# Kernel tuning notes

Measured on AMD Instinct MI355X. Metric: run time of the kernel, lower is better.

## Reference

```python
import jax, jax.numpy as jnp
import numpy as np

B, T, D = 4, 2048, 1024
H = int(D * 8.0)          # SwiGLU hidden (ffn_ratio=8)
SPARSITY = 0.95
THRESHOLD = 0.05          # PLIF firing threshold
PLIF_TAU = 2.5            # PLIF tau init
ALPHA = 2.0               # atan surrogate sharpness
EPS = 1e-6


@jax.custom_vjp
def spike(x):
    # Heaviside in fwd; atan surrogate gradient in bwd.
    return (x > 0).astype(x.dtype)

def _spike_fwd(x):
    return spike(x), x

def _spike_bwd(x, g):
    return (g * (ALPHA / 2.0) / (1.0 + (jnp.pi / 2.0 * ALPHA * x) ** 2),)

spike.defvjp(_spike_fwd, _spike_bwd)


def rmsnorm(x, w):
    return x * jax.lax.rsqrt(jnp.mean(x * x, axis=-1, keepdims=True) + EPS) * w


def setup_inputs() -> dict:
    key = jax.random.key(0)
    ks = jax.random.split(key, 12)
    f32 = jnp.float32
    return {
        "x": jax.random.normal(ks[0], (B, T, D), f32),
        "ln1_w": jnp.ones((D,), f32),
        "liq_win": (jax.random.normal(ks[1], (D, D), f32) / np.float32(np.sqrt(D))),
        "liq_wrec": (jax.random.normal(ks[2], (D, D), f32) / np.float32(np.sqrt(D))),
        "liq_b": jnp.zeros((D,), f32),
        "liq_tau": jnp.ones((D,), f32),  # softplus -> per-unit time constant
        "plif_w": jnp.asarray(-np.log(PLIF_TAU - 1.0), f32),  # sigmoid(w)=1/tau
        "syn_w": jax.random.normal(ks[3], (D, D), f32) * 0.02,
        "gate_w": jax.random.normal(ks[4], (D, D), f32) * 0.01,
        "gate_b": jnp.zeros((D,), f32),
        "ln2_w": jnp.ones((D,), f32),
        "ffn_wg": jax.random.normal(ks[5], (H, D), f32) * 0.02,
        "ffn_wu": jax.random.normal(ks[6], (H, D), f32) * 0.02,
        "ffn_wd": jax.random.normal(ks[7], (D, H), f32) * (0.02 / np.float32(np.sqrt(2.0))),
        "syn_mask": (jax.random.uniform(ks[8], (D, D)) > SPARSITY),  # bool, fixed
    }


def reference(x, ln1_w, liq_win, liq_wrec, liq_b, liq_tau, plif_w, syn_w,
              gate_w, gate_b, ln2_w, ffn_wg, ffn_wu, ffn_wd, syn_mask):
    # --- pre-norm ---
    a = rmsnorm(x, ln1_w)                       # (B,T,D)
    a_t = jnp.swapaxes(a, 0, 1)                 # (T,B,D)

    # --- LiquidCell: liquid time-constant recurrence over T ---
    tau = jax.nn.softplus(liq_tau)              # (D,) per-unit time constant

    def liq_step(h, xt):
        pre = xt @ liq_win.T + h @ liq_wrec.T + liq_b
        h = h + (jnp.tanh(pre) - h) / tau
        return h, h

    h0 = jnp.zeros((x.shape[0], D), x.dtype)
    _, h_seq = jax.lax.scan(liq_step, h0, a_t)  # (T,B,D)

    # --- PLIFCell.forward_seq: parametric LIF, subtract reset ---
    decay = jax.nn.sigmoid(plif_w)              # scalar = 1/tau_plif

    def plif_step(v, ht):
        v = v + decay * (ht - v)
        s = spike(v - THRESHOLD)
        v = v - s * THRESHOLD                   # reset='subtract'
        return v, s

    _, s_seq = jax.lax.scan(plif_step, jnp.zeros_like(h0), h_seq)
    s = jnp.swapaxes(s_seq, 0, 1)               # (B,T,D) spikes

    # --- SparseSynapse * sigmoid gate ---
    w_eff = syn_w * syn_mask.astype(syn_w.dtype)
    gated = (s @ w_eff.T) * jax.nn.sigmoid(s @ gate_w.T + gate_b)
    x = x + gated                               # dropout=0 -> identity

    # --- SwiGLU FFN residual ---
    y = rmsnorm(x, ln2_w)
    ff = (jax.nn.silu(y @ ffn_wg.T) * (y @ ffn_wu.T)) @ ffn_wd.T
    return x + ff
```

## Files before the change

kernel.cpp:

```cpp
#include <hip/hip_runtime.h>
#include <hip/hip_bf16.h>

#define TT 2048
#define DIM 1024
#define HFF 8192
#define NBATCH 4
#define PWG 32
#define THRESH 0.05f

typedef __bf16 bf16x8 __attribute__((ext_vector_type(8)));
typedef float f32x4 __attribute__((ext_vector_type(4)));

__device__ __forceinline__ unsigned short f2bf(float f) {
    __hip_bfloat16 h = __float2bfloat16(f);
    return __builtin_bit_cast(unsigned short, h);
}
__device__ __forceinline__ float bf2f(unsigned short u) {
    return __bfloat162float(__builtin_bit_cast(__hip_bfloat16, u));
}
__device__ __forceinline__ bf16x8 ldf(const unsigned short* p) {
    return *reinterpret_cast<const bf16x8*>(p);
}

__device__ __forceinline__ void ld2x4_mall(const float* p0, const float* p1,
                                           f32x4* a, f32x4* b) {
    asm volatile("global_load_dwordx4 %0, %2, off sc0 sc1\n\t"
                 "global_load_dwordx4 %1, %3, off sc0 sc1\n\t"
                 "s_waitcnt vmcnt(0)"
                 : "=&v"(*a), "=&v"(*b) : "v"(p0), "v"(p1) : "memory");
}

__device__ __forceinline__ void gload_lds16(const void* g, void* l) {
    __builtin_amdgcn_global_load_lds(
        (const __attribute__((address_space(1))) unsigned int*)g,
        (__attribute__((address_space(3))) unsigned int*)l, 16, 0, 0);
}

__global__ void maskprobe_k(const unsigned int* mask_words, int* flag) {
    __shared__ int allok;
    if (threadIdx.x == 0) allok = 1;
    __syncthreads();
    int ok = 1;
    for (int i = 0; i < 16; ++i) {
        unsigned int w = mask_words[threadIdx.x * 16 + i];
        if (w > 1u) ok = 0;
    }
    if (!ok) atomicAnd(&allok, 0);
    __syncthreads();
    if (threadIdx.x == 0) flag[0] = allok;
}

__global__ void weff_k(const float* __restrict__ synw, const void* __restrict__ mask,
                       const int* __restrict__ flag, unsigned short* __restrict__ dst) {
    const int isInt = flag[0];
    const int n = DIM * DIM;
    for (int i = blockIdx.x * 256 + threadIdx.x; i < n; i += gridDim.x * 256) {
        bool m;
        if (isInt) m = ((const int*)mask)[i] != 0;
        else       m = ((const unsigned char*)mask)[i] != 0;
        dst[i] = f2bf(m ? synw[i] : 0.f);
    }
}

__global__ void conv_k(const float* __restrict__ src, unsigned short* __restrict__ dst, int n) {
    for (int i = blockIdx.x * 256 + threadIdx.x; i < n; i += gridDim.x * 256)
        dst[i] = f2bf(src[i]);
}

__global__ void split_k(const float* __restrict__ src, unsigned short* __restrict__ hi,
                        unsigned short* __restrict__ lo, int n) {
    for (int i = blockIdx.x * 256 + threadIdx.x; i < n; i += gridDim.x * 256) {
        float v = src[i];
        unsigned short h = f2bf(v);
        hi[i] = h;
        lo[i] = f2bf(v - bf2f(h));
    }
}

__global__ void spkexp_k(const unsigned int* __restrict__ spk, unsigned short* __restrict__ sbf) {
    const int i = blockIdx.x * 256 + threadIdx.x;
    const unsigned int w = spk[i];
    const int d = i & 1023, t32 = (i >> 10) & 63, b = i >> 16;
    const size_t base = ((size_t)b * TT + (size_t)t32 * 32) * DIM + d;
    #pragma unroll
    for (int j = 0; j < 32; ++j)
        sbf[base + (size_t)j * DIM] = ((w >> j) & 1u) ? (unsigned short)0x3F80 : (unsigned short)0;
}

template <bool SPLIT>
__global__ void rms_k(const float* __restrict__ xin, const float* __restrict__ w,
                      unsigned short* __restrict__ hi, unsigned short* __restrict__ lo) {
    const int row = blockIdx.x;
    const int tid = threadIdx.x;
    const float4 xv = *reinterpret_cast<const float4*>(xin + (size_t)row * DIM + tid * 4);
    float ss = xv.x * xv.x + xv.y * xv.y + xv.z * xv.z + xv.w * xv.w;
    #pragma unroll
    for (int m = 1; m <= 32; m <<= 1) ss += __shfl_xor(ss, m);
    __shared__ float red[5];
    if ((tid & 63) == 0) red[tid >> 6] = ss;
    __syncthreads();
    if (tid == 0) {
        float s = red[0] + red[1] + red[2] + red[3];
        red[4] = 1.f / sqrtf(s * (1.f / DIM) + 1e-6f);
    }
    __syncthreads();
    const float scale = red[4];
    const float wv[4] = {w[tid*4], w[tid*4+1], w[tid*4+2], w[tid*4+3]};
    const float xa[4] = {xv.x, xv.y, xv.z, xv.w};
    #pragma unroll
    for (int i = 0; i < 4; ++i) {
        float v = xa[i] * scale * wv[i];
        unsigned short h = f2bf(v);
        hi[(size_t)row * DIM + tid * 4 + i] = h;
        if constexpr (SPLIT) lo[(size_t)row * DIM + tid * 4 + i] = f2bf(v - bf2f(h));
    }
}

template <int EPI>
__global__ __launch_bounds__(256, 1) void gemm2_k(
    const unsigned short* __restrict__ A,  const unsigned short* __restrict__ Alo,
    const unsigned short* __restrict__ B1, const unsigned short* __restrict__ B1lo,
    const unsigned short* __restrict__ B2,
    const float* __restrict__ aux1, const float* __restrict__ aux2,
    float* __restrict__ outf, unsigned short* __restrict__ outbf,
    int N, int K) {
    constexpr bool HILO = (EPI == 0);
    constexpr bool DUAL = (EPI == 1 || EPI == 2);
    __shared__ unsigned short sA[128 * 64];
    __shared__ unsigned short sB1[128 * 64];
    __shared__ unsigned short sAlo[HILO ? 128 * 64 : 8];
    __shared__ unsigned short sBlo[HILO ? 128 * 64 : 8];
    __shared__ unsigned short sB2[DUAL ? 128 * 64 : 8];
    const int lane = threadIdx.x & 63;
    const int wv = threadIdx.x >> 6;
    const int l15 = lane & 15, l4 = lane >> 4;
    const long row0 = (long)blockIdx.y * 128;
    const long col0 = (long)blockIdx.x * 128;
    const int wr = wv >> 1, wc = wv & 1;
    const int crow = lane >> 3;
    const int cbyte = (lane & 7) * 16;
    f32x4 acc[4][4];
    f32x4 acc2[DUAL ? 4 : 1][DUAL ? 4 : 1];
    #pragma unroll
    for (int i = 0; i < 4; ++i)
        #pragma unroll
        for (int j = 0; j < 4; ++j) {
            acc[i][j] = (f32x4){0.f, 0.f, 0.f, 0.f};
            if constexpr (DUAL) acc2[i][j] = (f32x4){0.f, 0.f, 0.f, 0.f};
        }
    for (int kt = 0; kt < K; kt += 64) {
        #pragma unroll
        for (int i = 0; i < 4; ++i) {
            const int chunk = wv * 4 + i;
            const int trow = chunk * 8 + crow;
            const size_t goffA = ((row0 + trow) * (size_t)K + kt) * 2 + cbyte;
            const size_t goffB = ((col0 + trow) * (size_t)K + kt) * 2 + cbyte;
            gload_lds16((const char*)A + goffA, (char*)sA + chunk * 1024);
            gload_lds16((const char*)B1 + goffB, (char*)sB1 + chunk * 1024);
            if constexpr (HILO) {
                gload_lds16((const char*)Alo + goffA, (char*)sAlo + chunk * 1024);
                gload_lds16((const char*)B1lo + goffB, (char*)sBlo + chunk * 1024);
            }
            if constexpr (DUAL)
                gload_lds16((const char*)B2 + goffB, (char*)sB2 + chunk * 1024);
        }
        __syncthreads();
        #pragma unroll
        for (int kk2 = 0; kk2 < 64; kk2 += 32) {
            bf16x8 af[4], bf_[4], al[4], bl[4], b2f[4];
            #pragma unroll
            for (int i = 0; i < 4; ++i) {
                const int ao = (wr * 64 + i * 16 + l15) * 64 + kk2 + l4 * 8;
                const int bo = (wc * 64 + i * 16 + l15) * 64 + kk2 + l4 * 8;
                af[i]  = ldf(sA + ao);
                bf_[i] = ldf(sB1 + bo);
                if constexpr (HILO) { al[i] = ldf(sAlo + ao); bl[i] = ldf(sBlo + bo); }
                if constexpr (DUAL) b2f[i] = ldf(sB2 + bo);
            }
            #pragma unroll
            for (int i = 0; i < 4; ++i)
                #pragma unroll
                for (int j = 0; j < 4; ++j) {
                    acc[i][j] = __builtin_amdgcn_mfma_f32_16x16x32_bf16(af[i], bf_[j], acc[i][j], 0, 0, 0);
                    if constexpr (HILO) {
                        acc[i][j] = __builtin_amdgcn_mfma_f32_16x16x32_bf16(af[i], bl[j], acc[i][j], 0, 0, 0);
                        acc[i][j] = __builtin_amdgcn_mfma_f32_16x16x32_bf16(al[i], bf_[j], acc[i][j], 0, 0, 0);
                    }
                    if constexpr (DUAL)
                        acc2[i][j] = __builtin_amdgcn_mfma_f32_16x16x32_bf16(af[i], b2f[j], acc2[i][j], 0, 0, 0);
                }
        }
        __syncthreads();
    }
    #pragma unroll
    for (int i = 0; i < 4; ++i) {
        #pragma unroll
        for (int r = 0; r < 4; ++r) {
            const long row = row0 + wr * 64 + i * 16 + l4 * 4 + r;
            #pragma unroll
            for (int j = 0; j < 4; ++j) {
                const long col = col0 + wc * 64 + j * 16 + l15;
                float v = acc[i][j][r];
                if constexpr (EPI == 0) {
                    int m = (int)row;
                    int bb = m >> 11, tt = m & 2047;
                    outf[((size_t)(tt * NBATCH + bb)) * DIM + col] = v + aux1[col];
                } else if constexpr (EPI == 1) {
                    size_t idx = (size_t)row * N + col;
                    float gg = acc2[i][j][r] + aux2[col];
                    outf[idx] = aux1[idx] + v * (1.f / (1.f + expf(-gg)));
                } else if constexpr (EPI == 2) {
                    size_t idx = (size_t)row * N + col;
                    float u = acc2[i][j][r];
                    outbf[idx] = f2bf((v / (1.f + expf(-v))) * u);
                } else {
                    size_t idx = (size_t)row * N + col;
                    outf[idx] = aux1[idx] + v;
                }
            }
        }
    }
}

__global__ __launch_bounds__(512, 1) void recur_k(
    const float* __restrict__ wrec, const float* __restrict__ U,
    const float* __restrict__ liqtau, const float* __restrict__ plifw,
    float* __restrict__ hg, int* __restrict__ flags, unsigned int* __restrict__ spk) {
    const int tid = threadIdx.x;
    const int wg = blockIdx.x;
    const int g = tid >> 6;
    const int L = tid & 63;
    const int kp = L;
    const int d0 = wg * 32 + g * 4;

    float wreg[4][16];
    #pragma unroll
    for (int d = 0; d < 4; ++d) {
        const float* wr = wrec + (size_t)(d0 + d) * DIM + kp * 16;
        #pragma unroll
        for (int q = 0; q < 4; ++q) {
            f32x4 w4 = *reinterpret_cast<const f32x4*>(wr + q * 4);
            wreg[d][q*4+0] = w4[0]; wreg[d][q*4+1] = w4[1];
            wreg[d][q*4+2] = w4[2]; wreg[d][q*4+3] = w4[3];
        }
    }

    __shared__ float hl[4 * 1088];
    for (int i = tid; i < 4 * 1088; i += 512) hl[i] = 0.f;

    const int od = L >> 2, ob = L & 3;
    const int odim = d0 + od;
    const bool own = (L < 16);
    float hq = 0.f, vq = 0.f, tauv = 1.f;
    unsigned smask = 0u;
    const float decay = 1.f / (1.f + expf(-plifw[0]));
    if (own) {
        float lt = liqtau[odim];
        tauv = (lt > 20.f) ? lt : log1pf(expf(lt));
    }
    const int sel1 = L & 1, sel2 = (L >> 1) & 1, sel4 = (L >> 2) & 1, sel8 = (L >> 3) & 1;

    int cb[4];
    #pragma unroll
    for (int b = 0; b < 4; ++b)
        cb[b] = b * 1088 + (kp >> 2) * 68 + (kp & 3) * 16;
    __syncthreads();

    for (int t = 0; t < TT; ++t) {
        float uvp = 0.f;
        if (own) uvp = U[((size_t)t * NBATCH + ob) * DIM + odim];

        float a[16];
        #pragma unroll
        for (int v = 0; v < 16; ++v) a[v] = 0.f;
        #pragma unroll
        for (int q = 0; q < 4; ++q) {
            const f32x4 h0 = *reinterpret_cast<const f32x4*>(hl + cb[0] + q * 4);
            const f32x4 h1 = *reinterpret_cast<const f32x4*>(hl + cb[1] + q * 4);
            const f32x4 h2 = *reinterpret_cast<const f32x4*>(hl + cb[2] + q * 4);
            const f32x4 h3 = *reinterpret_cast<const f32x4*>(hl + cb[3] + q * 4);
            #pragma unroll
            for (int d = 0; d < 4; ++d)
                #pragma unroll
                for (int e = 0; e < 4; ++e) {
                    const float w = wreg[d][q * 4 + e];
                    a[d*4+0] = fmaf(w, h0[e], a[d*4+0]);
                    a[d*4+1] = fmaf(w, h1[e], a[d*4+1]);
                    a[d*4+2] = fmaf(w, h2[e], a[d*4+2]);
                    a[d*4+3] = fmaf(w, h3[e], a[d*4+3]);
                }
        }
        #pragma unroll
        for (int j = 0; j < 8; ++j) {
            float snd = sel1 ? a[2*j] : a[2*j+1];
            float kept = sel1 ? a[2*j+1] : a[2*j];
            a[j] = kept + __shfl_xor(snd, 1);
        }
        #pragma unroll
        for (int j = 0; j < 4; ++j) {
            float snd = sel2 ? a[2*j] : a[2*j+1];
            float kept = sel2 ? a[2*j+1] : a[2*j];
            a[j] = kept + __shfl_xor(snd, 2);
        }
        #pragma unroll
        for (int j = 0; j < 2; ++j) {
            float snd = sel4 ? a[2*j] : a[2*j+1];
            float kept = sel4 ? a[2*j+1] : a[2*j];
            a[j] = kept + __shfl_xor(snd, 4);
        }
        {
            float snd = sel8 ? a[0] : a[1];
            float kept = sel8 ? a[1] : a[0];
            a[0] = kept + __shfl_xor(snd, 8);
        }
        a[0] += __shfl_xor(a[0], 16);
        a[0] += __shfl_xor(a[0], 32);

        if (own) {
            float pre = a[0] + uvp;
            float th = tanhf(pre);
            float hn = hq + (th - hq) / tauv;
            hq = hn;
            float v = vq + decay * (hn - vq);
            float s = ((v - THRESH) > 0.f) ? 1.f : 0.f;
            vq = v - s * THRESH;
            smask |= (s > 0.f ? 1u : 0u) << (t & 31);
            if ((t & 31) == 31) {
                __hip_atomic_store(&spk[ob * 65536 + (t >> 5) * 1024 + odim], smask,
                                   __ATOMIC_RELAXED, __HIP_MEMORY_SCOPE_SYSTEM);
                smask = 0u;
            }
            __hip_atomic_store(&hg[(size_t)(t & 1) * 4096 + ob * 1024 + odim], hn,
                               __ATOMIC_RELAXED, __HIP_MEMORY_SCOPE_SYSTEM);
        }
        if (t == TT - 1) break;
        __syncthreads();
        if (tid == 0)
            __hip_atomic_store(&flags[wg], t + 1, __ATOMIC_RELAXED, __HIP_MEMORY_SCOPE_SYSTEM);
        if (g == 0) {
            while (__hip_atomic_load(&flags[L & 31], __ATOMIC_RELAXED,
                                     __HIP_MEMORY_SCOPE_SYSTEM) < t + 1) {}
        }
        __syncthreads();
        {
            const float* src = hg + (size_t)(t & 1) * 4096;
            const int b = tid >> 7, k0 = (tid & 127) * 8;
            const int w = b * 1088 + (k0 >> 6) * 68 + (k0 & 63);
            f32x4 va, vb;
            ld2x4_mall(src + b * 1024 + k0, src + b * 1024 + k0 + 4, &va, &vb);
            *reinterpret_cast<f32x4*>(hl + w) = va;
            *reinterpret_cast<f32x4*>(hl + w + 4) = vb;
        }
        __syncthreads();
    }
}

extern "C" void kernel_launch(void* const* d_in, const int* in_sizes, int n_in,
                              void* d_out, int out_size, void* d_ws, size_t ws_size,
                              hipStream_t stream) {
    (void)in_sizes; (void)n_in; (void)out_size;
    const float* x     = (const float*)d_in[0];
    const float* ln1   = (const float*)d_in[1];
    const float* win   = (const float*)d_in[2];
    const float* wrec  = (const float*)d_in[3];
    const float* liqb  = (const float*)d_in[4];
    const float* liqtau= (const float*)d_in[5];
    const float* plifw = (const float*)d_in[6];
    const float* synw  = (const float*)d_in[7];
    const float* gatew = (const float*)d_in[8];
    const float* gateb = (const float*)d_in[9];
    const float* ln2   = (const float*)d_in[10];
    const float* wgp   = (const float*)d_in[11];
    const float* wup   = (const float*)d_in[12];
    const float* wdp   = (const float*)d_in[13];
    const void*  mask  = d_in[14];
    float* dout = (float*)d_out;
    char* ws = (char*)d_ws;
    const size_t MB = (size_t)1 << 20;

    unsigned short* winh  = (unsigned short*)(ws + 0 * MB);
    unsigned short* winl  = (unsigned short*)(ws + 2 * MB);
    unsigned short* weffb = (unsigned short*)(ws + 4 * MB);
    unsigned short* gatewb= (unsigned short*)(ws + 6 * MB);
    unsigned short* wgb   = (unsigned short*)(ws + 8 * MB);
    unsigned short* wub   = (unsigned short*)(ws + 24 * MB);
    unsigned short* wdb   = (unsigned short*)(ws + 40 * MB);
    unsigned short* ahi   = (unsigned short*)(ws + 56 * MB);
    unsigned short* alo   = (unsigned short*)(ws + 72 * MB);
    float*          Ubuf  = (float*)(ws + 88 * MB);
    unsigned short* hffb  = (unsigned short*)(ws + 88 * MB);
    unsigned short* sbf   = (unsigned short*)(ws + 120 * MB);
    float*          x2    = (float*)(ws + 136 * MB);
    float*          hgb   = (float*)(ws + 168 * MB);
    int*            flags = (int*)(ws + 168 * MB + 64 * 1024);
    int*            flag  = (int*)(ws + 168 * MB + 80 * 1024);
    unsigned int*   spk   = (unsigned int*)(ws + 169 * MB);
    unsigned short* hfull = (unsigned short*)(ws + 171 * MB);
    const bool FULLFFN = (ws_size >= 306 * MB);

    hipMemsetAsync(flags, 0, 512, stream);
    maskprobe_k<<<1, 256, 0, stream>>>((const unsigned int*)mask, flag);
    weff_k<<<1024, 256, 0, stream>>>(synw, mask, flag, weffb);
    split_k<<<1024, 256, 0, stream>>>(win, winh, winl, DIM * DIM);
    conv_k<<<1024, 256, 0, stream>>>(gatew, gatewb, DIM * DIM);
    conv_k<<<2048, 256, 0, stream>>>(wgp, wgb, HFF * DIM);
    conv_k<<<2048, 256, 0, stream>>>(wup, wub, HFF * DIM);
    conv_k<<<2048, 256, 0, stream>>>(wdp, wdb, DIM * HFF);

    rms_k<true><<<NBATCH * TT, 256, 0, stream>>>(x, ln1, ahi, alo);
    gemm2_k<0><<<dim3(DIM / 128, (NBATCH * TT) / 128), 256, 0, stream>>>(
        ahi, alo, winh, winl, nullptr, liqb, nullptr, Ubuf, nullptr, DIM, DIM);

    recur_k<<<PWG, 512, 0, stream>>>(wrec, Ubuf, liqtau, plifw, hgb, flags, spk);
    spkexp_k<<<(NBATCH * 64 * 1024) / 256, 256, 0, stream>>>(spk, sbf);

    gemm2_k<1><<<dim3(DIM / 128, (NBATCH * TT) / 128), 256, 0, stream>>>(
        sbf, nullptr, weffb, nullptr, gatewb, x, gateb, x2, nullptr, DIM, DIM);

    rms_k<false><<<NBATCH * TT, 256, 0, stream>>>(x2, ln2, ahi, nullptr);

    if (FULLFFN) {
        gemm2_k<2><<<dim3(HFF / 128, (NBATCH * TT) / 128), 256, 0, stream>>>(
            ahi, nullptr, wgb, nullptr, wub, nullptr, nullptr,
            nullptr, hfull, HFF, DIM);
        gemm2_k<3><<<dim3(DIM / 128, (NBATCH * TT) / 128), 256, 0, stream>>>(
            hfull, nullptr, wdb, nullptr, nullptr, x2, nullptr,
            dout, nullptr, DIM, HFF);
    } else {
        const int CH = 2048;
        for (int c = 0; c < (NBATCH * TT) / CH; ++c) {
            const size_t ro = (size_t)c * CH;
            gemm2_k<2><<<dim3(HFF / 128, CH / 128), 256, 0, stream>>>(
                ahi + ro * DIM, nullptr, wgb, nullptr, wub, nullptr, nullptr,
                nullptr, hffb, HFF, DIM);
            gemm2_k<3><<<dim3(DIM / 128, CH / 128), 256, 0, stream>>>(
                hffb, nullptr, wdb, nullptr, nullptr, x2 + ro * DIM, nullptr,
                dout + ro * DIM, nullptr, DIM, HFF);
        }
    }
}
```

Baseline: 7.783 ms.

## Split recurrence workgroups by batch pairs to double persistent recurrence parallelism

The persistent recurrence kernel now runs 64 workgroups instead of 32, with each workgroup handling the same 32 output dimensions but only two of the four batch rows. Per-step FMA work, LDS footprint and hidden-state reload per workgroup are halved, and the shuffle reduction tree is shortened. In exchange the weight rows are duplicated across two workgroups and the cross-workgroup flag barrier spins on 64 flags each timestep, which adds synchronisation latency to a loop that is already latency-bound.

```diff
diff --git a/kernel.cpp b/kernel.cpp
--- a/kernel.cpp
+++ b/kernel.cpp
@@ -5,7 +5,7 @@
 #define DIM 1024
 #define HFF 8192
 #define NBATCH 4
-#define PWG 32
+#define PWG 64
 #define THRESH 0.05f
 
 typedef __bf16 bf16x8 __attribute__((ext_vector_type(8)));
@@ -22,12 +22,10 @@
     return *reinterpret_cast<const bf16x8*>(p);
 }
 
-__device__ __forceinline__ void ld2x4_mall(const float* p0, const float* p1,
-                                           f32x4* a, f32x4* b) {
-    asm volatile("global_load_dwordx4 %0, %2, off sc0 sc1\n\t"
-                 "global_load_dwordx4 %1, %3, off sc0 sc1\n\t"
+__device__ __forceinline__ void ld1x4_mall(const float* p, f32x4* a) {
+    asm volatile("global_load_dwordx4 %0, %1, off sc0 sc1\n\t"
                  "s_waitcnt vmcnt(0)"
-                 : "=&v"(*a), "=&v"(*b) : "v"(p0), "v"(p1) : "memory");
+                 : "=&v"(*a) : "v"(p) : "memory");
 }
 
 __device__ __forceinline__ void gload_lds16(const void* g, void* l) {
@@ -231,7 +229,8 @@
     const int g = tid >> 6;
     const int L = tid & 63;
     const int kp = L;
-    const int d0 = wg * 32 + g * 4;
+    const int d0 = (wg >> 1) * 32 + g * 4;
+    const int bp = (wg & 1) * 2;
 
     float wreg[4][16];
     #pragma unroll
@@ -245,12 +244,13 @@
         }
     }
 
-    __shared__ float hl[4 * 1088];
-    for (int i = tid; i < 4 * 1088; i += 512) hl[i] = 0.f;
-
-    const int od = L >> 2, ob = L & 3;
+    __shared__ float hl[2 * 1088];
+    for (int i = tid; i < 2 * 1088; i += 512) hl[i] = 0.f;
+
+    const int od = L >> 1, obl = L & 1;
+    const int ob = bp + obl;
     const int odim = d0 + od;
-    const bool own = (L < 16);
+    const bool own = (L < 8);
     float hq = 0.f, vq = 0.f, tauv = 1.f;
     unsigned smask = 0u;
     const float decay = 1.f / (1.f + expf(-plifw[0]));
@@ -258,61 +258,54 @@
         float lt = liqtau[odim];
         tauv = (lt > 20.f) ? lt : log1pf(expf(lt));
     }
-    const int sel1 = L & 1, sel2 = (L >> 1) & 1, sel4 = (L >> 2) & 1, sel8 = (L >> 3) & 1;
-
-    int cb[4];
-    #pragma unroll
-    for (int b = 0; b < 4; ++b)
+    const int sel1 = L & 1, sel2 = (L >> 1) & 1, sel4 = (L >> 2) & 1;
+
+    int cb[2];
+    #pragma unroll
+    for (int b = 0; b < 2; ++b)
         cb[b] = b * 1088 + (kp >> 2) * 68 + (kp & 3) * 16;
+    const int rbb = tid >> 8, rk0 = (tid & 255) * 4;
+    const int rw = rbb * 1088 + (rk0 >> 6) * 68 + (rk0 & 63);
     __syncthreads();
 
     for (int t = 0; t < TT; ++t) {
         float uvp = 0.f;
         if (own) uvp = U[((size_t)t * NBATCH + ob) * DIM + odim];
 
-        float a[16];
-        #pragma unroll
-        for (int v = 0; v < 16; ++v) a[v] = 0.f;
+        float a[8];
+        #pragma unroll
+        for (int v = 0; v < 8; ++v) a[v] = 0.f;
         #pragma unroll
         for (int q = 0; q < 4; ++q) {
             const f32x4 h0 = *reinterpret_cast<const f32x4*>(hl + cb[0] + q * 4);
             const f32x4 h1 = *reinterpret_cast<const f32x4*>(hl + cb[1] + q * 4);
-            const f32x4 h2 = *reinterpret_cast<const f32x4*>(hl + cb[2] + q * 4);
-            const f32x4 h3 = *reinterpret_cast<const f32x4*>(hl + cb[3] + q * 4);
             #pragma unroll
             for (int d = 0; d < 4; ++d)
                 #pragma unroll
                 for (int e = 0; e < 4; ++e) {
                     const float w = wreg[d][q * 4 + e];
-                    a[d*4+0] = fmaf(w, h0[e], a[d*4+0]);
-                    a[d*4+1] = fmaf(w, h1[e], a[d*4+1]);
-                    a[d*4+2] = fmaf(w, h2[e], a[d*4+2]);
-                    a[d*4+3] = fmaf(w, h3[e], a[d*4+3]);
+                    a[d*2+0] = fmaf(w, h0[e], a[d*2+0]);
+                    a[d*2+1] = fmaf(w, h1[e], a[d*2+1]);
                 }
         }
         #pragma unroll
-        for (int j = 0; j < 8; ++j) {
+        for (int j = 0; j < 4; ++j) {
             float snd = sel1 ? a[2*j] : a[2*j+1];
             float kept = sel1 ? a[2*j+1] : a[2*j];
             a[j] = kept + __shfl_xor(snd, 1);
         }
         #pragma unroll
-        for (int j = 0; j < 4; ++j) {
+        for (int j = 0; j < 2; ++j) {
             float snd = sel2 ? a[2*j] : a[2*j+1];
             float kept = sel2 ? a[2*j+1] : a[2*j];
             a[j] = kept + __shfl_xor(snd, 2);
         }
-        #pragma unroll
-        for (int j = 0; j < 2; ++j) {
-            float snd = sel4 ? a[2*j] : a[2*j+1];
-            float kept = sel4 ? a[2*j+1] : a[2*j];
-            a[j] = kept + __shfl_xor(snd, 4);
-        }
         {
-            float snd = sel8 ? a[0] : a[1];
-            float kept = sel8 ? a[1] : a[0];
-            a[0] = kept + __shfl_xor(snd, 8);
-        }
+            float snd = sel4 ? a[0] : a[1];
+            float kept = sel4 ? a[1] : a[0];
+            a[0] = kept + __shfl_xor(snd, 4);
+        }
+        a[0] += __shfl_xor(a[0], 8);
         a[0] += __shfl_xor(a[0], 16);
         a[0] += __shfl_xor(a[0], 32);
 
@@ -338,18 +331,15 @@
         if (tid == 0)
             __hip_atomic_store(&flags[wg], t + 1, __ATOMIC_RELAXED, __HIP_MEMORY_SCOPE_SYSTEM);
         if (g == 0) {
-            while (__hip_atomic_load(&flags[L & 31], __ATOMIC_RELAXED,
+            while (__hip_atomic_load(&flags[L], __ATOMIC_RELAXED,
                                      __HIP_MEMORY_SCOPE_SYSTEM) < t + 1) {}
         }
         __syncthreads();
         {
-            const float* src = hg + (size_t)(t & 1) * 4096;
-            const int b = tid >> 7, k0 = (tid & 127) * 8;
-            const int w = b * 1088 + (k0 >> 6) * 68 + (k0 & 63);
-            f32x4 va, vb;
-            ld2x4_mall(src + b * 1024 + k0, src + b * 1024 + k0 + 4, &va, &vb);
-            *reinterpret_cast<f32x4*>(hl + w) = va;
-            *reinterpret_cast<f32x4*>(hl + w + 4) = vb;
+            const float* src = hg + (size_t)(t & 1) * 4096 + (bp + rbb) * 1024 + rk0;
+            f32x4 va;
+            ld1x4_mall(src, &va);
+            *reinterpret_cast<f32x4*>(hl + rw) = va;
         }
         __syncthreads();
     }
@@ -398,7 +388,7 @@
     unsigned short* hfull = (unsigned short*)(ws + 171 * MB);
     const bool FULLFFN = (ws_size >= 306 * MB);
 
-    hipMemsetAsync(flags, 0, 512, stream);
+    hipMemsetAsync(flags, 0, 1024, stream);
     maskprobe_k<<<1, 256, 0, stream>>>((const unsigned int*)mask, flag);
     weff_k<<<1024, 256, 0, stream>>>(synw, mask, flag, weffb);
     split_k<<<1024, 256, 0, stream>>>(win, winh, winl, DIM * DIM);
```

After: 9.120 ms. +17.2%, slower.
